# Optimization experiments

Measured on AMD Instinct MI355X. Metric: run time of the kernel, lower is better.

The kernel has to match this reference:

```python
import jax, jax.numpy as jnp
import numpy as np

N_WIRES = 8
DIM = 1 << N_WIRES  # 256

# --- static precompute: CNOT-ring basis permutation and PauliZ sign matrix ---
# torchquantum convention: wire 0 is the most significant bit of the basis index.
_gates = [(w, w + 1) for w in range(N_WIRES - 1)] + [(N_WIRES - 1, 0)]
_perm = np.empty(DIM, dtype=np.int64)
for b in range(DIM):
    bits = [(b >> (N_WIRES - 1 - w)) & 1 for w in range(N_WIRES)]
    for c, t in _gates:
        if bits[c]:
            bits[t] ^= 1
    _perm[b] = sum(bit << (N_WIRES - 1 - w) for w, bit in enumerate(bits))
_Z = np.array([[1.0 - 2.0 * ((idx >> (N_WIRES - 1 - w)) & 1) for w in range(N_WIRES)]
               for idx in range(DIM)], dtype=np.float32)
# exp_Z[w] = sum_b probs_in[b] * Z[perm[b], w]  (CNOTs permute basis states)
_M = jnp.asarray(_Z[_perm])  # [256, 8]


def _quantum_head(angles):
    """angles: [..., 8] RX angles -> PauliZ expectations [..., 8].

    Circuit: RX(angle_w) on each wire from |0>, CNOT ring, MeasureAll(PauliZ).
    Post-RX state is a product state; CNOTs only permute basis states, so
    probabilities suffice (no complex amplitudes needed).
    """
    half = angles * 0.5
    c2 = jnp.cos(half) ** 2  # P(qubit=0)
    s2 = jnp.sin(half) ** 2  # P(qubit=1)
    # Build the 256-dim joint probability vector via sequential outer products.
    p = jnp.ones(angles.shape[:-1] + (1,), angles.dtype)
    for w in range(N_WIRES):
        pw = jnp.stack([c2[..., w], s2[..., w]], axis=-1)  # [..., 2]
        p = (p[..., :, None] * pw[..., None, :]).reshape(angles.shape[:-1] + (-1,))
    return p @ _M.astype(p.dtype)  # [..., 8]


def setup_inputs() -> dict:
    key = jax.random.key(0)
    ks = jax.random.split(key, 6)
    B, S, E = 8, 512, 768
    scale = 1.0 / np.sqrt(E)
    return {
        "x": jax.random.normal(ks[0], (B, S, E), jnp.float32),
        "W_proj": jax.random.normal(ks[1], (E, E), jnp.float32) * scale,
        "b_proj": jax.random.normal(ks[2], (E,), jnp.float32) * 0.02,
        "theta": jax.random.normal(ks[3], (N_WIRES,), jnp.float32),
        "W_comb": jax.random.normal(ks[4], (E, E), jnp.float32) * scale,
        "b_comb": jax.random.normal(ks[5], (E,), jnp.float32) * 0.02,
    }


def reference(x, W_proj, b_proj, theta, W_comb, b_comb):
    B, S, E = x.shape
    H = E // N_WIRES  # num_heads = 96
    proj = x @ W_proj.T + b_proj                 # [B, S, E] (torch Linear)
    angles = proj.reshape(B, S, H, N_WIRES) + theta  # encoder RX(x) then RX(theta): angles add
    expz = _quantum_head(angles)                 # [B, S, H, 8]
    out = expz.reshape(B, S, E)                  # heads re-concatenated
    # dropout is identity in eval mode
    return out @ W_comb.T + b_comb
```

## Files before the change

kernel.cpp:

```cpp
#include <hip/hip_runtime.h>

typedef _Float16 v8h __attribute__((ext_vector_type(8)));
typedef float    v4f __attribute__((ext_vector_type(4)));

__device__ __forceinline__ void gl_lds16(const void* g, void* l) {
  __builtin_amdgcn_global_load_lds(
      (__attribute__((address_space(1))) void*)(void*)g,
      (__attribute__((address_space(3))) void*)l, 16, 0, 0);
}
__device__ __forceinline__ v8h cvt8(const float4 a, const float4 b) {
  v8h o;
  o[0] = (_Float16)a.x; o[1] = (_Float16)a.y; o[2] = (_Float16)a.z; o[3] = (_Float16)a.w;
  o[4] = (_Float16)b.x; o[5] = (_Float16)b.y; o[6] = (_Float16)b.z; o[7] = (_Float16)b.w;
  return o;
}

__global__ void conv_w(const float4* __restrict__ wp, const float4* __restrict__ wc,
                       v8h* __restrict__ op, v8h* __restrict__ oc) {
  const int n = 73728;
  int i = blockIdx.x * blockDim.x + threadIdx.x;
  const float4* src = (i < n) ? wp : wc;
  v8h* dst = (i < n) ? op : oc;
  const int j = (i < n) ? i : i - n;
  dst[j] = cvt8(src[2 * j], src[2 * j + 1]);
}


__global__ __launch_bounds__(256) void gemm1_qh(
    const float* __restrict__ X,
    const _Float16* __restrict__ B,
    const float* __restrict__ bp,
    const float* __restrict__ theta,
    _Float16* __restrict__ EZ) {
  const int t = threadIdx.x;
  const int b = blockIdx.x;
  const int xcd = b & 7, slot = b >> 3;
  const int bm = xcd * 8 + slot / 12;
  const int bn = slot % 12;

  const int wave = t >> 6, lane = t & 63;
  const int quad = lane >> 4, l16 = lane & 15;
  const int wm = (wave >> 1) * 32, wn = (wave & 1) * 32;

  __shared__ __align__(16) unsigned char smem[32768];
  _Float16* As = (_Float16*)smem;
  _Float16* Bs = (_Float16*)(smem + 16384);
  float* Cs = (float*)smem;

  const float4 th0 = *(const float4*)theta;
  const float4 th1 = *(const float4*)(theta + 4);

  const int tr = t >> 4;
  const int tc = t & 15;
  const int cgl = tc ^ tr;

  const float*    Xg = X + (size_t)(bm * 64 + tr) * 768 + cgl * 8;
  const _Float16* Bg = B + (size_t)(bn * 64 + tr) * 768 + cgl * 8;

  v4f acc[2][2];
#pragma unroll
  for (int i = 0; i < 2; i++)
#pragma unroll
    for (int j = 0; j < 2; j++) acc[i][j] = (v4f){0.f, 0.f, 0.f, 0.f};

  for (int kt = 0; kt < 768; kt += 128) {
#pragma unroll
    for (int c = 0; c < 4; c++)
      gl_lds16(Bg + (size_t)c * 16 * 768 + kt, &Bs[c * 2048 + t * 8]);
#pragma unroll
    for (int c = 0; c < 4; c++) {
      const float* p = Xg + (size_t)c * 16 * 768 + kt;
      const float4 a0 = *(const float4*)p;
      const float4 a1 = *(const float4*)(p + 4);
      *(v8h*)&As[c * 2048 + t * 8] = cvt8(a0, a1);
    }
    __syncthreads();
#pragma unroll
    for (int q = 0; q < 4; q++) {
      v8h af[2], bf[2];
#pragma unroll
      for (int i = 0; i < 2; i++)
        af[i] = *(const v8h*)&As[(wm + i * 16 + l16) * 128 + (((q * 4 + quad) ^ l16) * 8)];
#pragma unroll
      for (int j = 0; j < 2; j++)
        bf[j] = *(const v8h*)&Bs[(wn + j * 16 + l16) * 128 + (((q * 4 + quad) ^ l16) * 8)];
#pragma unroll
      for (int i = 0; i < 2; i++)
#pragma unroll
        for (int j = 0; j < 2; j++)
          acc[i][j] = __builtin_amdgcn_mfma_f32_16x16x32_f16(af[i], bf[j], acc[i][j], 0, 0, 0);
    }
    __syncthreads();
  }

  const int r0 = wm + quad * 4;
  const int c0 = wn + l16;
#pragma unroll
  for (int j = 0; j < 2; j++)
#pragma unroll
    for (int i = 0; i < 2; i++)
#pragma unroll
      for (int r = 0; r < 4; r++)
        Cs[(r0 + i * 16 + r) * 68 + c0 + j * 16] = acc[i][j][r];
  __syncthreads();

#pragma unroll
  for (int s = 0; s < 2; s++) {
    const int idx = t + s * 256;
    const int row = idx >> 3, h = idx & 7;
    const int gcol = bn * 64 + h * 8;
    const float* cr = &Cs[row * 68 + h * 8];
    const float4 q0 = *(const float4*)cr;
    const float4 q1 = *(const float4*)(cr + 4);
    const float4 b0 = *(const float4*)(bp + gcol);
    const float4 b1 = *(const float4*)(bp + gcol + 4);
    float c[8];
    c[0] = cosf(q0.x + b0.x + th0.x);
    c[1] = cosf(q0.y + b0.y + th0.y);
    c[2] = cosf(q0.z + b0.z + th0.z);
    c[3] = cosf(q0.w + b0.w + th0.w);
    c[4] = cosf(q1.x + b1.x + th1.x);
    c[5] = cosf(q1.y + b1.y + th1.y);
    c[6] = cosf(q1.z + b1.z + th1.z);
    c[7] = cosf(q1.w + b1.w + th1.w);
    float e[8];
    e[0] = c[1] * c[2] * c[3] * c[4] * c[5] * c[6] * c[7];
    float pr = c[0];
#pragma unroll
    for (int w = 1; w < 8; w++) { pr *= c[w]; e[w] = pr; }
    v8h ov;
#pragma unroll
    for (int w = 0; w < 8; w++) ov[w] = (_Float16)e[w];
    *(v8h*)(EZ + (size_t)(bm * 64 + row) * 768 + gcol) = ov;
  }
}

__global__ __launch_bounds__(256) void gemm2(
    const _Float16* __restrict__ A,
    const _Float16* __restrict__ B,
    float* __restrict__ C,
    const float* __restrict__ bias) {
  const int t = threadIdx.x;
  const int b = blockIdx.x;
  const int xcd = b & 7, slot = b >> 3;
  const int bm = xcd * 8 + slot / 12;
  const int bn = slot % 12;

  const int wave = t >> 6, lane = t & 63;
  const int quad = lane >> 4, l16 = lane & 15;
  const int wm = (wave >> 1) * 32, wn = (wave & 1) * 32;

  __shared__ __align__(16) _Float16 Bs[64 * 128];

  const int tr = t >> 4;
  const int tc = t & 15;
  const int cgl = tc ^ tr;
  const _Float16* Bg = B + (size_t)(bn * 64 + tr) * 768 + cgl * 8;

  const _Float16* Ar0 = A + (size_t)(bm * 64 + wm + l16) * 768 + quad * 8;
  const _Float16* Ar1 = Ar0 + (size_t)16 * 768;

  v4f acc[2][2];
#pragma unroll
  for (int i = 0; i < 2; i++)
#pragma unroll
    for (int j = 0; j < 2; j++) acc[i][j] = (v4f){0.f, 0.f, 0.f, 0.f};

  for (int kt = 0; kt < 768; kt += 128) {
#pragma unroll
    for (int c = 0; c < 4; c++)
      gl_lds16(Bg + (size_t)c * 16 * 768 + kt, &Bs[c * 2048 + t * 8]);
    __syncthreads();
#pragma unroll
    for (int q = 0; q < 4; q++) {
      v8h af[2], bf[2];
      af[0] = *(const v8h*)(Ar0 + kt + q * 32);
      af[1] = *(const v8h*)(Ar1 + kt + q * 32);
#pragma unroll
      for (int j = 0; j < 2; j++)
        bf[j] = *(const v8h*)&Bs[(wn + j * 16 + l16) * 128 + (((q * 4 + quad) ^ l16) * 8)];
#pragma unroll
      for (int ii = 0; ii < 2; ii++)
#pragma unroll
        for (int j = 0; j < 2; j++)
          acc[ii][j] = __builtin_amdgcn_mfma_f32_16x16x32_f16(af[ii], bf[j], acc[ii][j], 0, 0, 0);
    }
    __syncthreads();
  }

  const int row0 = bm * 64 + wm + quad * 4;
  const int col0 = bn * 64 + wn + l16;
#pragma unroll
  for (int j = 0; j < 2; j++) {
    const int col = col0 + j * 16;
    const float bv = bias[col];
#pragma unroll
    for (int i = 0; i < 2; i++) {
#pragma unroll
      for (int r = 0; r < 4; r++) {
        C[(size_t)(row0 + i * 16 + r) * 768 + col] = acc[i][j][r] + bv;
      }
    }
  }
}

extern "C" void kernel_launch(void* const* d_in, const int* in_sizes, int n_in,
                              void* d_out, int out_size, void* d_ws, size_t ws_size,
                              hipStream_t stream) {
  const float* x     = (const float*)d_in[0];
  const float* Wp    = (const float*)d_in[1];
  const float* bp    = (const float*)d_in[2];
  const float* theta = (const float*)d_in[3];
  const float* Wcf   = (const float*)d_in[4];
  const float* bc    = (const float*)d_in[5];
  float* out = (float*)d_out;

  const size_t EE = (size_t)768 * 768;

  _Float16* WPH = (_Float16*)d_ws;
  _Float16* WCH = WPH + EE;
  _Float16* EZ  = WCH + EE;

  conv_w<<<(int)(2 * EE / 8 / 256), 256, 0, stream>>>(
      (const float4*)Wp, (const float4*)Wcf, (v8h*)WPH, (v8h*)WCH);

  gemm1_qh<<<768, 256, 0, stream>>>(x, WPH, bp, theta, EZ);

  gemm2<<<768, 256, 0, stream>>>(EZ, WCH, out, bc);
}
```

Before: 111.4 us.

## Prefetch X tiles into registers in gemm1 and stage A through LDS in gemm2

In gemm1, the next k-tile of X is loaded into registers right after the barrier, so the global load overlaps the MFMA work on the current tile instead of stalling before the LDS store. In gemm2, the A operand now arrives through swizzled LDS using async global_load_lds, replacing direct strided global fragment loads per wave, which makes the loads coalesced. The cost is more registers in gemm1 (16 extra float4) and an extra 16KB of LDS per block in gemm2, which could lower occupancy.

Result: faster. 99.02 us, median of 2 (-11.1%).

```diff
diff --git a/kernel.cpp b/kernel.cpp
--- a/kernel.cpp
+++ b/kernel.cpp
@@ -63,18 +63,30 @@
 #pragma unroll
     for (int j = 0; j < 2; j++) acc[i][j] = (v4f){0.f, 0.f, 0.f, 0.f};
 
+  float4 xr[4][2];
+#pragma unroll
+  for (int c = 0; c < 4; c++) {
+    const float* p = Xg + (size_t)c * 16 * 768;
+    xr[c][0] = *(const float4*)p;
+    xr[c][1] = *(const float4*)(p + 4);
+  }
+
   for (int kt = 0; kt < 768; kt += 128) {
 #pragma unroll
     for (int c = 0; c < 4; c++)
       gl_lds16(Bg + (size_t)c * 16 * 768 + kt, &Bs[c * 2048 + t * 8]);
 #pragma unroll
-    for (int c = 0; c < 4; c++) {
-      const float* p = Xg + (size_t)c * 16 * 768 + kt;
-      const float4 a0 = *(const float4*)p;
-      const float4 a1 = *(const float4*)(p + 4);
-      *(v8h*)&As[c * 2048 + t * 8] = cvt8(a0, a1);
-    }
-    __syncthreads();
+    for (int c = 0; c < 4; c++)
+      *(v8h*)&As[c * 2048 + t * 8] = cvt8(xr[c][0], xr[c][1]);
+    __syncthreads();
+    if (kt + 128 < 768) {
+#pragma unroll
+      for (int c = 0; c < 4; c++) {
+        const float* p = Xg + (size_t)c * 16 * 768 + kt + 128;
+        xr[c][0] = *(const float4*)p;
+        xr[c][1] = *(const float4*)(p + 4);
+      }
+    }
 #pragma unroll
     for (int q = 0; q < 4; q++) {
       v8h af[2], bf[2];
@@ -150,16 +162,16 @@
   const int quad = lane >> 4, l16 = lane & 15;
   const int wm = (wave >> 1) * 32, wn = (wave & 1) * 32;
 
+  __shared__ __align__(16) _Float16 As[64 * 128];
   __shared__ __align__(16) _Float16 Bs[64 * 128];
 
   const int tr = t >> 4;
   const int tc = t & 15;
   const int cgl = tc ^ tr;
+
+  const _Float16* Ag = A + (size_t)(bm * 64 + tr) * 768 + cgl * 8;
   const _Float16* Bg = B + (size_t)(bn * 64 + tr) * 768 + cgl * 8;
 
-  const _Float16* Ar0 = A + (size_t)(bm * 64 + wm + l16) * 768 + quad * 8;
-  const _Float16* Ar1 = Ar0 + (size_t)16 * 768;
-
   v4f acc[2][2];
 #pragma unroll
   for (int i = 0; i < 2; i++)
@@ -168,14 +180,17 @@
 
   for (int kt = 0; kt < 768; kt += 128) {
 #pragma unroll
-    for (int c = 0; c < 4; c++)
+    for (int c = 0; c < 4; c++) {
+      gl_lds16(Ag + (size_t)c * 16 * 768 + kt, &As[c * 2048 + t * 8]);
       gl_lds16(Bg + (size_t)c * 16 * 768 + kt, &Bs[c * 2048 + t * 8]);
+    }
     __syncthreads();
 #pragma unroll
     for (int q = 0; q < 4; q++) {
       v8h af[2], bf[2];
-      af[0] = *(const v8h*)(Ar0 + kt + q * 32);
-      af[1] = *(const v8h*)(Ar1 + kt + q * 32);
+#pragma unroll
+      for (int i = 0; i < 2; i++)
+        af[i] = *(const v8h*)&As[(wm + i * 16 + l16) * 128 + (((q * 4 + quad) ^ l16) * 8)];
 #pragma unroll
       for (int j = 0; j < 2; j++)
         bf[j] = *(const v8h*)&Bs[(wn + j * 16 + l16) * 128 + (((q * 4 + quad) ^ l16) * 8)];
```
